# Kernel optimization log

Measured on AMD Instinct MI355X. Metric: run time of the kernel, lower is better.

## Reference

```python
import jax, jax.numpy as jnp
import numpy as np

N_NODES = 100000
N_EDGES = 1600000
D = 64


def setup_inputs() -> dict:
    key = jax.random.key(0)
    k0, k1, k2, k3 = jax.random.split(key, 4)
    x = jax.random.normal(k0, (N_NODES, D), dtype=jnp.float32)
    edge_index = jax.random.randint(k1, (2, N_EDGES), 0, N_NODES, dtype=jnp.int64)
    W1 = jax.random.normal(k2, (D, D), dtype=jnp.float32) * 0.1
    b1 = jnp.zeros((D,), dtype=jnp.float32)
    W2 = jax.random.normal(k3, (D, D), dtype=jnp.float32) * 0.1
    b2 = jnp.zeros((D,), dtype=jnp.float32)
    return {"x": x, "edge_index": edge_index, "W1": W1, "b1": b1, "W2": W2, "b2": b2}


def _gcn_layer(x, edge_index, W, b):
    n = x.shape[0]
    h = x @ W  # [N, Dout] -- transform before aggregation (small GEMM)
    loop = jnp.arange(n, dtype=edge_index.dtype)
    src = jnp.concatenate([edge_index[0], loop])
    dst = jnp.concatenate([edge_index[1], loop])
    deg = jax.ops.segment_sum(jnp.ones_like(dst, dtype=h.dtype), dst, num_segments=n)
    dinv = jax.lax.rsqrt(deg)  # deg >= 1 thanks to self loops
    norm = dinv[src] * dinv[dst]  # [E+N]
    msg = h[src] * norm[:, None]  # gather: [E+N, Dout]
    agg = jax.ops.segment_sum(msg, dst, num_segments=n)  # scatter-add
    return agg + b


def reference(x, edge_index, W1, b1, W2, b2):
    # dropout p = 0.0 -> identity
    h = jax.nn.relu(_gcn_layer(x, edge_index, W1, b1))
    h = jax.nn.relu(_gcn_layer(h, edge_index, W2, b2))
    return h
```

## Files before the change

### kernel.cpp

```cpp
#include <hip/hip_runtime.h>
#include <hip/hip_bf16.h>

#define D 64
#define NB_HIST 256
#define MAXBK 512
#define QSHIFT 14

typedef float vfloat4 __attribute__((ext_vector_type(4)));
typedef short short8 __attribute__((ext_vector_type(8)));
typedef float f32x4 __attribute__((ext_vector_type(4)));

__device__ __forceinline__ unsigned short f2bf(float f) {
    union { float f; unsigned u; } v; v.f = f;
    unsigned r = (v.u + 0x7FFF + ((v.u >> 16) & 1)) >> 16;
    return (unsigned short)r;
}
__device__ __forceinline__ unsigned short bftrunc(float f) {
    union { float f; unsigned u; } v; v.f = f;
    return (unsigned short)(v.u >> 16);
}
__device__ __forceinline__ float bffrom(unsigned short h) {
    union { unsigned u; float f; } v; v.u = ((unsigned)h) << 16; return v.f;
}
__device__ __forceinline__ float bflo(unsigned u) {
    union { unsigned u; float f; } v; v.u = u << 16; return v.f;
}
__device__ __forceinline__ float bfhi(unsigned u) {
    union { unsigned u; float f; } v; v.u = u & 0xFFFF0000u; return v.f;
}

__global__ __launch_bounds__(256) void passA_hist_wfrag(
    const int* __restrict__ dst, int* __restrict__ blockCounts, int E, int per, int NBK,
    const float* __restrict__ W1, const float* __restrict__ W2,
    unsigned short* __restrict__ WfH1, unsigned short* __restrict__ WfL1,
    unsigned short* __restrict__ WfH2, unsigned short* __restrict__ WfL2)
{
    int tid = threadIdx.x;

    if ((int)blockIdx.x < NB_HIST) {
        __shared__ int hist[MAXBK];
        for (int i = tid; i < NBK; i += 256) hist[i] = 0;
        __syncthreads();
        int lo = blockIdx.x * per, hi = min(E, lo + per);
        for (int i = lo + tid * 4; i < hi; i += 1024) {
            if (i + 3 < hi) {
                int4 d4 = *(const int4*)(dst + i);
                atomicAdd(&hist[d4.x >> 8], 1);
                atomicAdd(&hist[d4.y >> 8], 1);
                atomicAdd(&hist[d4.z >> 8], 1);
                atomicAdd(&hist[d4.w >> 8], 1);
            } else {
                for (int k = i; k < hi; ++k) atomicAdd(&hist[dst[k] >> 8], 1);
            }
        }
        __syncthreads();
        for (int i = tid; i < NBK; i += 256)
            blockCounts[(size_t)blockIdx.x * NBK + i] = hist[i];
        return;
    }

    int b = (int)blockIdx.x - NB_HIST;
    const float* Wsrc = (b >> 1) ? W2 : W1;
    unsigned short* fh = (b >> 1) ? WfH2 : WfH1;
    unsigned short* fl = (b >> 1) ? WfL2 : WfL1;
    int combo = (b & 1) * 4 + (tid >> 6);
    int lane = tid & 63;
    int s = combo >> 2, c = combo & 3, g = lane >> 4, rl = lane & 15;
#pragma unroll
    for (int j = 0; j < 8; ++j) {
        float v = Wsrc[(32 * s + 8 * g + j) * D + 16 * c + rl];
        unsigned short h = bftrunc(v);
        fh[combo * 512 + lane * 8 + j] = h;
        fl[combo * 512 + lane * 8 + j] = f2bf(v - bffrom(h));
    }
}

__global__ __launch_bounds__(256) void scan_cols(
    const int* __restrict__ blockCounts, int* __restrict__ partial,
    int* __restrict__ totals, int NBK)
{
    int wave = threadIdx.x >> 6, lane = threadIdx.x & 63;
    int k = blockIdx.x * 4 + wave;
    if (k >= NBK) return;
    int carry = 0;
    for (int base = 0; base < NB_HIST; base += 64) {
        int b = base + lane;
        int v = blockCounts[(size_t)b * NBK + k];
        int inc = v;
        for (int d = 1; d < 64; d <<= 1) {
            int t = __shfl_up(inc, d, 64);
            if (lane >= d) inc += t;
        }
        partial[(size_t)k * NB_HIST + b] = inc - v + carry;
        carry += __shfl(inc, 63, 64);
    }
    if (lane == 0) totals[k] = carry;
}

__global__ __launch_bounds__(256) void passB(
    const int* __restrict__ src, const int* __restrict__ dst,
    const int* __restrict__ totals, const int* __restrict__ partial,
    int* __restrict__ bucketed, int E, int per, int NBK)
{
    __shared__ int cur[MAXBK];
    __shared__ int sBofs[MAXBK];
    int tid = threadIdx.x, b = blockIdx.x;

    if (tid < 64) {
        int carry = 0;
        for (int base = 0; base < NBK; base += 64) {
            int i = base + tid;
            int v = (i < NBK) ? totals[i] : 0;
            int inc = v;
            for (int d = 1; d < 64; d <<= 1) {
                int t = __shfl_up(inc, d, 64);
                if (tid >= d) inc += t;
            }
            if (i < NBK) sBofs[i] = inc - v + carry;
            carry += __shfl(inc, 63, 64);
        }
    }
    __syncthreads();
    for (int i = tid; i < NBK; i += 256)
        cur[i] = sBofs[i] + partial[(size_t)i * NB_HIST + b];
    __syncthreads();

    int lo = b * per, hi = min(E, lo + per);
    for (int i = lo + tid * 4; i < hi; i += 1024) {
        if (i + 3 < hi) {
            int4 d4 = *(const int4*)(dst + i);
            int4 s4 = *(const int4*)(src + i);
            int p0 = atomicAdd(&cur[d4.x >> 8], 1);
            int p1 = atomicAdd(&cur[d4.y >> 8], 1);
            int p2 = atomicAdd(&cur[d4.z >> 8], 1);
            int p3 = atomicAdd(&cur[d4.w >> 8], 1);
            bucketed[p0] = (s4.x << 8) | (d4.x & 255);
            bucketed[p1] = (s4.y << 8) | (d4.y & 255);
            bucketed[p2] = (s4.z << 8) | (d4.z & 255);
            bucketed[p3] = (s4.w << 8) | (d4.w & 255);
        } else {
            for (int k = i; k < hi; ++k) {
                int d = dst[k], s = src[k];
                int pos = atomicAdd(&cur[d >> 8], 1);
                bucketed[pos] = (s << 8) | (d & 255);
            }
        }
    }
}

__global__ __launch_bounds__(256) void build_csr(
    const int* __restrict__ bucketed, const int* __restrict__ totals,
    int* __restrict__ deg, float* __restrict__ dinv,
    int* __restrict__ ofs, int* __restrict__ csr, int N)
{
    __shared__ int h8[256 * 8];
    __shared__ int scn[256];
    __shared__ int sE0;
    int tid = threadIdx.x, k = blockIdx.x;

    if (tid < 64) {
        int s = 0;
        for (int i = tid; i < k; i += 64) s += totals[i];
        for (int d = 32; d >= 1; d >>= 1) s += __shfl_xor(s, d, 64);
        if (tid == 0) sE0 = s;
    }
    for (int i = tid; i < 2048; i += 256) h8[i] = 0;
    __syncthreads();

    int e0 = sE0, e1 = e0 + totals[k];
    int node = k * 256 + tid;

    for (int i = e0 + tid; i < e1; i += 256) {
        int v = bucketed[i];
        atomicAdd(&h8[((v & 255) << 3) | ((unsigned)(v >> 8) >> QSHIFT)], 1);
    }
    __syncthreads();

    int c[8]; int mydeg = 0;
#pragma unroll
    for (int b = 0; b < 8; ++b) { c[b] = h8[tid * 8 + b]; mydeg += c[b]; }
    scn[tid] = mydeg;
    __syncthreads();
    for (int d2 = 1; d2 < 256; d2 <<= 1) {
        int t = (tid >= d2) ? scn[tid - d2] : 0;
        __syncthreads();
        scn[tid] += t;
        __syncthreads();
    }
    int myofs = scn[tid] - mydeg;

    if (node < N) {
        deg[node]  = mydeg;
        dinv[node] = rsqrtf((float)(mydeg + 1));
        ofs[node]  = e0 + myofs;
    }

    int run = myofs;
#pragma unroll
    for (int b = 0; b < 8; ++b) { h8[tid * 8 + b] = run; run += c[b]; }
    __syncthreads();
    for (int i = e0 + tid; i < e1; i += 256) {
        int v = bucketed[i];
        int s = v >> 8;
        int pos = atomicAdd(&h8[((v & 255) << 3) | ((unsigned)s >> QSHIFT)], 1);
        csr[e0 + pos] = s;
    }
}

__global__ __launch_bounds__(256) void gemm1_mfma(
    const float* __restrict__ X,
    const unsigned short* __restrict__ WfH, const unsigned short* __restrict__ WfL,
    const float* __restrict__ dinv, unsigned short* __restrict__ hn, int N)
{
    int t = threadIdx.x, wave = t >> 6, lane = t & 63;
    int rowBase = (int)blockIdx.x * 64 + wave * 16;
    if (rowBase >= N) return;
    int g = lane >> 4, rl = lane & 15;

    short8 BH[2][4], BL[2][4];
#pragma unroll
    for (int s = 0; s < 2; ++s)
#pragma unroll
        for (int c = 0; c < 4; ++c) {
            BH[s][c] = *(const short8*)(WfH + ((s * 4 + c) * 64 + lane) * 8);
            BL[s][c] = *(const short8*)(WfL + ((s * 4 + c) * 64 + lane) * 8);
        }

    int arow = rowBase + rl; if (arow >= N) arow = N - 1;
    const float* xr = X + (size_t)arow * D;

    f32x4 acc[4];
#pragma unroll
    for (int c = 0; c < 4; ++c) acc[c] = (f32x4){0.f, 0.f, 0.f, 0.f};

#pragma unroll
    for (int s = 0; s < 2; ++s) {
        vfloat4 x0 = *(const vfloat4*)(xr + 32 * s + 8 * g);
        vfloat4 x1 = *(const vfloat4*)(xr + 32 * s + 8 * g + 4);
        short8 ah, al;
#pragma unroll
        for (int j = 0; j < 4; ++j) {
            unsigned short h0 = bftrunc(x0[j]);
            ah[j] = (short)h0; al[j] = (short)f2bf(x0[j] - bffrom(h0));
            unsigned short h1 = bftrunc(x1[j]);
            ah[j + 4] = (short)h1; al[j + 4] = (short)f2bf(x1[j] - bffrom(h1));
        }
#pragma unroll
        for (int c = 0; c < 4; ++c)
            acc[c] = __builtin_amdgcn_mfma_f32_16x16x32_bf16(ah, BH[s][c], acc[c], 0, 0, 0);
#pragma unroll
        for (int c = 0; c < 4; ++c)
            acc[c] = __builtin_amdgcn_mfma_f32_16x16x32_bf16(ah, BL[s][c], acc[c], 0, 0, 0);
#pragma unroll
        for (int c = 0; c < 4; ++c)
            acc[c] = __builtin_amdgcn_mfma_f32_16x16x32_bf16(al, BH[s][c], acc[c], 0, 0, 0);
    }

#pragma unroll
    for (int r = 0; r < 4; ++r) {
        int row = rowBase + g * 4 + r;
        if (row < N) {
            float dv = dinv[row];
            unsigned short* hr = hn + (size_t)row * D + rl;
#pragma unroll
            for (int c = 0; c < 4; ++c) hr[c * 16] = f2bf(acc[c][r] * dv);
        }
    }
}

__global__ __launch_bounds__(256) void agg1_gemm2(
    const int* __restrict__ ofs, const int* __restrict__ deg,
    const int* __restrict__ csr, const unsigned short* __restrict__ hnA,
    const float* __restrict__ dinv, const float* __restrict__ bias,
    const unsigned short* __restrict__ WfH, const unsigned short* __restrict__ WfL,
    unsigned short* __restrict__ hnB, int N)
{
    __shared__ unsigned short sH[32 * 72];
    int tid  = threadIdx.x;
    int lane = tid & 63, wave = tid >> 6;
    int grp  = lane >> 3, sub = lane & 7;
    int rowInBlk = wave * 8 + grp;
    int nodeBase = (int)blockIdx.x * 32;
    int node = nodeBase + rowInBlk;
    bool live = (node < N);

    const int4* hrow = (const int4*)hnA;
    float2 a0 = {0.f, 0.f}, a1 = {0.f, 0.f}, a2 = {0.f, 0.f}, a3 = {0.f, 0.f};

    int s0 = 0, cnt = 0;
    if (live) {
        s0  = ofs[node];
        cnt = deg[node];
        int4 h = hrow[(size_t)node * 8 + sub];
        a0.x += bflo(h.x); a0.y += bfhi(h.x);
        a1.x += bflo(h.y); a1.y += bfhi(h.y);
        a2.x += bflo(h.z); a2.y += bfhi(h.z);
        a3.x += bflo(h.w); a3.y += bfhi(h.w);
    }

    const int* cp = csr + s0;
    int j = 0;
    for (; j + 3 < cnt; j += 4) {
        int sA = cp[j], sB = cp[j + 1], sC = cp[j + 2], sD = cp[j + 3];
        int4 hA = hrow[(size_t)sA * 8 + sub];
        int4 hB = hrow[(size_t)sB * 8 + sub];
        int4 hC = hrow[(size_t)sC * 8 + sub];
        int4 hD = hrow[(size_t)sD * 8 + sub];
        a0.x += bflo(hA.x); a0.y += bfhi(hA.x);
        a1.x += bflo(hA.y); a1.y += bfhi(hA.y);
        a2.x += bflo(hA.z); a2.y += bfhi(hA.z);
        a3.x += bflo(hA.w); a3.y += bfhi(hA.w);
        a0.x += bflo(hB.x); a0.y += bfhi(hB.x);
        a1.x += bflo(hB.y); a1.y += bfhi(hB.y);
        a2.x += bflo(hB.z); a2.y += bfhi(hB.z);
        a3.x += bflo(hB.w); a3.y += bfhi(hB.w);
        a0.x += bflo(hC.x); a0.y += bfhi(hC.x);
        a1.x += bflo(hC.y); a1.y += bfhi(hC.y);
        a2.x += bflo(hC.z); a2.y += bfhi(hC.z);
        a3.x += bflo(hC.w); a3.y += bfhi(hC.w);
        a0.x += bflo(hD.x); a0.y += bfhi(hD.x);
        a1.x += bflo(hD.y); a1.y += bfhi(hD.y);
        a2.x += bflo(hD.z); a2.y += bfhi(hD.z);
        a3.x += bflo(hD.w); a3.y += bfhi(hD.w);
    }
    for (; j < cnt; ++j) {
        int sA = cp[j];
        int4 hA = hrow[(size_t)sA * 8 + sub];
        a0.x += bflo(hA.x); a0.y += bfhi(hA.x);
        a1.x += bflo(hA.y); a1.y += bfhi(hA.y);
        a2.x += bflo(hA.z); a2.y += bfhi(hA.z);
        a3.x += bflo(hA.w); a3.y += bfhi(hA.w);
    }

    {
        float dw = live ? dinv[node] : 0.f;
        float4 b0 = ((const float4*)bias)[sub * 2];
        float4 b1 = ((const float4*)bias)[sub * 2 + 1];
        float o0 = fmaxf(a0.x * dw + b0.x, 0.f);
        float o1 = fmaxf(a0.y * dw + b0.y, 0.f);
        float o2 = fmaxf(a1.x * dw + b0.z, 0.f);
        float o3 = fmaxf(a1.y * dw + b0.w, 0.f);
        float o4 = fmaxf(a2.x * dw + b1.x, 0.f);
        float o5 = fmaxf(a2.y * dw + b1.y, 0.f);
        float o6 = fmaxf(a3.x * dw + b1.z, 0.f);
        float o7 = fmaxf(a3.y * dw + b1.w, 0.f);
        unsigned r0 = (unsigned)f2bf(o0) | ((unsigned)f2bf(o1) << 16);
        unsigned r1 = (unsigned)f2bf(o2) | ((unsigned)f2bf(o3) << 16);
        unsigned r2 = (unsigned)f2bf(o4) | ((unsigned)f2bf(o5) << 16);
        unsigned r3 = (unsigned)f2bf(o6) | ((unsigned)f2bf(o7) << 16);
        *(int4*)&sH[rowInBlk * 72 + sub * 8] = make_int4((int)r0, (int)r1, (int)r2, (int)r3);
    }
    __syncthreads();

    if (wave < 2) {
        int g = lane >> 4, rl = lane & 15;
        f32x4 acc[4];
#pragma unroll
        for (int c = 0; c < 4; ++c) acc[c] = (f32x4){0.f, 0.f, 0.f, 0.f};

#pragma unroll
        for (int s = 0; s < 2; ++s) {
            short8 a = *(const short8*)&sH[(wave * 16 + rl) * 72 + 32 * s + 8 * g];
            short8 BH[4], BL[4];
#pragma unroll
            for (int c = 0; c < 4; ++c) {
                BH[c] = *(const short8*)(WfH + ((s * 4 + c) * 64 + lane) * 8);
                BL[c] = *(const short8*)(WfL + ((s * 4 + c) * 64 + lane) * 8);
            }
#pragma unroll
            for (int c = 0; c < 4; ++c)
                acc[c] = __builtin_amdgcn_mfma_f32_16x16x32_bf16(a, BH[c], acc[c], 0, 0, 0);
#pragma unroll
            for (int c = 0; c < 4; ++c)
                acc[c] = __builtin_amdgcn_mfma_f32_16x16x32_bf16(a, BL[c], acc[c], 0, 0, 0);
        }

#pragma unroll
        for (int r = 0; r < 4; ++r) {
            int row = nodeBase + wave * 16 + g * 4 + r;
            if (row < N) {
                float dv = dinv[row];
                unsigned short* hw = hnB + (size_t)row * D + rl;
#pragma unroll
                for (int c = 0; c < 4; ++c) hw[c * 16] = f2bf(acc[c][r] * dv);
            }
        }
    }
}

__global__ __launch_bounds__(256) void aggregate_relu_f32(
    const int* __restrict__ ofs, const int* __restrict__ deg,
    const int* __restrict__ csr, const unsigned short* __restrict__ hn,
    const float* __restrict__ dinv, const float* __restrict__ bias,
    float* __restrict__ outF, int N)
{
    int t    = blockIdx.x * 256 + threadIdx.x;
    int lane = threadIdx.x & 63;
    int grp  = lane >> 3, sub = lane & 7;
    int node = (t >> 6) * 8 + grp;
    bool live = (node < N);

    const int4* hrow = (const int4*)hn;
    float2 a0 = {0.f, 0.f}, a1 = {0.f, 0.f}, a2 = {0.f, 0.f}, a3 = {0.f, 0.f};

    int s0 = 0, cnt = 0;
    if (live) {
        s0  = ofs[node];
        cnt = deg[node];
        int4 h = hrow[(size_t)node * 8 + sub];
        a0.x += bflo(h.x); a0.y += bfhi(h.x);
        a1.x += bflo(h.y); a1.y += bfhi(h.y);
        a2.x += bflo(h.z); a2.y += bfhi(h.z);
        a3.x += bflo(h.w); a3.y += bfhi(h.w);
    }

    const int* cp = csr + s0;
    int j = 0;
    for (; j + 3 < cnt; j += 4) {
        int sA = cp[j], sB = cp[j + 1], sC = cp[j + 2], sD = cp[j + 3];
        int4 hA = hrow[(size_t)sA * 8 + sub];
        int4 hB = hrow[(size_t)sB * 8 + sub];
        int4 hC = hrow[(size_t)sC * 8 + sub];
        int4 hD = hrow[(size_t)sD * 8 + sub];
        a0.x += bflo(hA.x); a0.y += bfhi(hA.x);
        a1.x += bflo(hA.y); a1.y += bfhi(hA.y);
        a2.x += bflo(hA.z); a2.y += bfhi(hA.z);
        a3.x += bflo(hA.w); a3.y += bfhi(hA.w);
        a0.x += bflo(hB.x); a0.y += bfhi(hB.x);
        a1.x += bflo(hB.y); a1.y += bfhi(hB.y);
        a2.x += bflo(hB.z); a2.y += bfhi(hB.z);
        a3.x += bflo(hB.w); a3.y += bfhi(hB.w);
        a0.x += bflo(hC.x); a0.y += bfhi(hC.x);
        a1.x += bflo(hC.y); a1.y += bfhi(hC.y);
        a2.x += bflo(hC.z); a2.y += bfhi(hC.z);
        a3.x += bflo(hC.w); a3.y += bfhi(hC.w);
        a0.x += bflo(hD.x); a0.y += bfhi(hD.x);
        a1.x += bflo(hD.y); a1.y += bfhi(hD.y);
        a2.x += bflo(hD.z); a2.y += bfhi(hD.z);
        a3.x += bflo(hD.w); a3.y += bfhi(hD.w);
    }
    for (; j < cnt; ++j) {
        int sA = cp[j];
        int4 hA = hrow[(size_t)sA * 8 + sub];
        a0.x += bflo(hA.x); a0.y += bfhi(hA.x);
        a1.x += bflo(hA.y); a1.y += bfhi(hA.y);
        a2.x += bflo(hA.z); a2.y += bfhi(hA.z);
        a3.x += bflo(hA.w); a3.y += bfhi(hA.w);
    }

    if (live) {
        float dw = dinv[node];
        float4 b0 = ((const float4*)bias)[sub * 2];
        float4 b1 = ((const float4*)bias)[sub * 2 + 1];
        float o0 = fmaxf(a0.x * dw + b0.x, 0.f);
        float o1 = fmaxf(a0.y * dw + b0.y, 0.f);
        float o2 = fmaxf(a1.x * dw + b0.z, 0.f);
        float o3 = fmaxf(a1.y * dw + b0.w, 0.f);
        float o4 = fmaxf(a2.x * dw + b1.x, 0.f);
        float o5 = fmaxf(a2.y * dw + b1.y, 0.f);
        float o6 = fmaxf(a3.x * dw + b1.z, 0.f);
        float o7 = fmaxf(a3.y * dw + b1.w, 0.f);
        float4 v0 = make_float4(o0, o1, o2, o3);
        float4 v1 = make_float4(o4, o5, o6, o7);
        ((float4*)outF)[(size_t)node * 16 + sub * 2]     = v0;
        ((float4*)outF)[(size_t)node * 16 + sub * 2 + 1] = v1;
    }
}


extern "C" void kernel_launch(void* const* d_in, const int* in_sizes, int n_in,
                              void* d_out, int out_size, void* d_ws, size_t ws_size,
                              hipStream_t stream) {
    const float* x   = (const float*)d_in[0];
    const int*   ei  = (const int*)d_in[1];
    const float* W1  = (const float*)d_in[2];
    const float* b1  = (const float*)d_in[3];
    const float* W2  = (const float*)d_in[4];
    const float* b2  = (const float*)d_in[5];

    int N = in_sizes[0] / D;
    int E = in_sizes[1] / 2;
    const int* src = ei;
    const int* dst = ei + E;
    int NBK = (N + 255) >> 8;
    int per = (((E + NB_HIST - 1) / NB_HIST) + 3) & ~3;

    char* ws = (char*)d_ws;
    int*            blockCounts = (int*)(ws + 0x00000000);
    int*            partial     = (int*)(ws + 0x00080000);
    int*            totals      = (int*)(ws + 0x00100000);
    int*            deg         = (int*)(ws + 0x00120000);
    float*          dinv        = (float*)(ws + 0x00190000);
    int*            ofs         = (int*)(ws + 0x00200000);
    int*            bucketed    = (int*)(ws + 0x00280000);
    int*            csr         = (int*)(ws + 0x00A00000);
    unsigned short* hnA         = (unsigned short*)(ws + 0x01100000);
    unsigned short* hnB         = (unsigned short*)(ws + 0x01D80000);
    unsigned short* WfH1        = (unsigned short*)(ws + 0x02A80000);
    unsigned short* WfL1        = WfH1 + 4096;
    unsigned short* WfH2        = WfL1 + 4096;
    unsigned short* WfL2        = WfH2 + 4096;
    float*          outF        = (float*)d_out;

    int nb_G = (N + 63) / 64;
    int nb_A = (N + 31) / 32;

    passA_hist_wfrag<<<NB_HIST + 4, 256, 0, stream>>>(dst, blockCounts, E, per, NBK,
                                                      W1, W2, WfH1, WfL1, WfH2, WfL2);
    scan_cols<<<(NBK + 3) / 4, 256, 0, stream>>>(blockCounts, partial, totals, NBK);
    passB<<<NB_HIST, 256, 0, stream>>>(src, dst, totals, partial, bucketed, E, per, NBK);
    build_csr<<<NBK, 256, 0, stream>>>(bucketed, totals, deg, dinv, ofs, csr, N);

    gemm1_mfma<<<nb_G, 256, 0, stream>>>(x, WfH1, WfL1, dinv, hnA, N);
    agg1_gemm2<<<nb_A, 256, 0, stream>>>(ofs, deg, csr, hnA, dinv, b1, WfH2, WfL2, hnB, N);
    aggregate_relu_f32<<<nb_A, 256, 0, stream>>>(ofs, deg, csr, hnB, dinv, b2, outF, N);
}
```

Baseline: 199.0 us.

## Sort nodes by degree via permutation to balance aggregation waves

Builds a degree histogram in build_csr, scans it, and scatters node ids into a degree-sorted permutation. Both aggregation kernels then process nodes in permuted order, so the nodes sharing a wave have similar neighbor counts and less divergence. This adds two small kernels, a memset, and heavily contended atomics on a few degree bins. Output row accesses also become non-contiguous.

```diff
diff --git a/kernel.cpp b/kernel.cpp
--- a/kernel.cpp
+++ b/kernel.cpp
@@ -151,7 +151,7 @@
 __global__ __launch_bounds__(256) void build_csr(
     const int* __restrict__ bucketed, const int* __restrict__ totals,
     int* __restrict__ deg, float* __restrict__ dinv,
-    int* __restrict__ ofs, int* __restrict__ csr, int N)
+    int* __restrict__ ofs, int* __restrict__ csr, int* __restrict__ dhist, int N)
 {
     __shared__ int h8[256 * 8];
     __shared__ int scn[256];
@@ -193,6 +193,7 @@
         deg[node]  = mydeg;
         dinv[node] = rsqrtf((float)(mydeg + 1));
         ofs[node]  = e0 + myofs;
+        atomicAdd(&dhist[min(mydeg, 63)], 1);
     }
 
     int run = myofs;
@@ -207,6 +208,28 @@
     }
 }
 
+__global__ void perm_scan(const int* __restrict__ dhist, int* __restrict__ dcur) {
+    int lane = threadIdx.x;
+    int v = dhist[lane];
+    int inc = v;
+    for (int d = 1; d < 64; d <<= 1) {
+        int t = __shfl_up(inc, d, 64);
+        if (lane >= d) inc += t;
+    }
+    dcur[lane] = inc - v;
+}
+
+__global__ __launch_bounds__(256) void perm_scatter(
+    const int* __restrict__ deg, int* __restrict__ dcur, int* __restrict__ perm, int N)
+{
+    int i = (int)blockIdx.x * 256 + threadIdx.x;
+    if (i < N) {
+        int d = min(deg[i], 63);
+        int pos = atomicAdd(&dcur[d], 1);
+        perm[pos] = i;
+    }
+}
+
 __global__ __launch_bounds__(256) void gemm1_mfma(
     const float* __restrict__ X,
     const unsigned short* __restrict__ WfH, const unsigned short* __restrict__ WfL,
@@ -269,6 +292,7 @@
 }
 
 __global__ __launch_bounds__(256) void agg1_gemm2(
+    const int* __restrict__ perm,
     const int* __restrict__ ofs, const int* __restrict__ deg,
     const int* __restrict__ csr, const unsigned short* __restrict__ hnA,
     const float* __restrict__ dinv, const float* __restrict__ bias,
@@ -276,13 +300,15 @@
     unsigned short* __restrict__ hnB, int N)
 {
     __shared__ unsigned short sH[32 * 72];
+    __shared__ int sNid[32];
     int tid  = threadIdx.x;
     int lane = tid & 63, wave = tid >> 6;
     int grp  = lane >> 3, sub = lane & 7;
     int rowInBlk = wave * 8 + grp;
-    int nodeBase = (int)blockIdx.x * 32;
-    int node = nodeBase + rowInBlk;
-    bool live = (node < N);
+    int idx = (int)blockIdx.x * 32 + rowInBlk;
+    bool live = (idx < N);
+    int node = live ? perm[idx] : -1;
+    if (sub == 0) sNid[rowInBlk] = node;
 
     const int4* hrow = (const int4*)hnA;
     float2 a0 = {0.f, 0.f}, a1 = {0.f, 0.f}, a2 = {0.f, 0.f}, a3 = {0.f, 0.f};
@@ -377,10 +403,11 @@
 
 #pragma unroll
         for (int r = 0; r < 4; ++r) {
-            int row = nodeBase + wave * 16 + g * 4 + r;
-            if (row < N) {
-                float dv = dinv[row];
-                unsigned short* hw = hnB + (size_t)row * D + rl;
+            int rr = wave * 16 + g * 4 + r;
+            int nid = sNid[rr];
+            if (nid >= 0) {
+                float dv = dinv[nid];
+                unsigned short* hw = hnB + (size_t)nid * D + rl;
 #pragma unroll
                 for (int c = 0; c < 4; ++c) hw[c * 16] = f2bf(acc[c][r] * dv);
             }
@@ -389,6 +416,7 @@
 }
 
 __global__ __launch_bounds__(256) void aggregate_relu_f32(
+    const int* __restrict__ perm,
     const int* __restrict__ ofs, const int* __restrict__ deg,
     const int* __restrict__ csr, const unsigned short* __restrict__ hn,
     const float* __restrict__ dinv, const float* __restrict__ bias,
@@ -397,8 +425,9 @@
     int t    = blockIdx.x * 256 + threadIdx.x;
     int lane = threadIdx.x & 63;
     int grp  = lane >> 3, sub = lane & 7;
-    int node = (t >> 6) * 8 + grp;
-    bool live = (node < N);
+    int idx  = (t >> 6) * 8 + grp;
+    bool live = (idx < N);
+    int node = live ? perm[idx] : -1;
 
     const int4* hrow = (const int4*)hn;
     float2 a0 = {0.f, 0.f}, a1 = {0.f, 0.f}, a2 = {0.f, 0.f}, a3 = {0.f, 0.f};
@@ -500,18 +529,25 @@
     unsigned short* WfL1        = WfH1 + 4096;
     unsigned short* WfH2        = WfL1 + 4096;
     unsigned short* WfL2        = WfH2 + 4096;
+    int*            dhist       = (int*)(ws + 0x02A90000);
+    int*            dcur        = (int*)(ws + 0x02A90400);
+    int*            perm        = (int*)(ws + 0x02B00000);
     float*          outF        = (float*)d_out;
 
     int nb_G = (N + 63) / 64;
     int nb_A = (N + 31) / 32;
 
+    hipMemsetAsync(dhist, 0, 256, stream);
     passA_hist_wfrag<<<NB_HIST + 4, 256, 0, stream>>>(dst, blockCounts, E, per, NBK,
                                                       W1, W2, WfH1, WfL1, WfH2, WfL2);
     scan_cols<<<(NBK + 3) / 4, 256, 0, stream>>>(blockCounts, partial, totals, NBK);
     passB<<<NB_HIST, 256, 0, stream>>>(src, dst, totals, partial, bucketed, E, per, NBK);
-    build_csr<<<NBK, 256, 0, stream>>>(bucketed, totals, deg, dinv, ofs, csr, N);
+    build_csr<<<NBK, 256, 0, stream>>>(bucketed, totals, deg, dinv, ofs, csr, dhist, N);
+
+    perm_scan<<<1, 64, 0, stream>>>(dhist, dcur);
+    perm_scatter<<<(N + 255) / 256, 256, 0, stream>>>(deg, dcur, perm, N);
 
     gemm1_mfma<<<nb_G, 256, 0, stream>>>(x, WfH1, WfL1, dinv, hnA, N);
-    agg1_gemm2<<<nb_A, 256, 0, stream>>>(ofs, deg, csr, hnA, dinv, b1, WfH2, WfL2, hnB, N);
-    aggregate_relu_f32<<<nb_A, 256, 0, stream>>>(ofs, deg, csr, hnB, dinv, b2, outF, N);
-}
+    agg1_gemm2<<<nb_A, 256, 0, stream>>>(perm, ofs, deg, csr, hnA, dinv, b1, WfH2, WfL2, hnB, N);
+    aggregate_relu_f32<<<nb_A, 256, 0, stream>>>(perm, ofs, deg, csr, hnB, dinv, b2, outF, N);
+}
```

After: 728.8 us. 3.66x slower.
